# Kernel tuning notes

Measured on AMD Instinct MI355X. Metric: run time of the kernel, lower is better.

The kernel has to match this reference:

```python
import jax, jax.numpy as jnp
import numpy as np
from jax import lax

N_CLASS = 21          # VOC: 20 foreground + background
SCORE_THRESH = 0.05   # 'evaluate' preset
NMS_THRESH = 0.3


def loc2bbox(src_bbox, loc):
    # src_bbox, loc: [N, 4] in (y1, x1, y2, x2) / (dy, dx, dh, dw)
    h = src_bbox[:, 2] - src_bbox[:, 0]
    w = src_bbox[:, 3] - src_bbox[:, 1]
    cy = src_bbox[:, 0] + 0.5 * h
    cx = src_bbox[:, 1] + 0.5 * w
    dy, dx, dh, dw = loc[:, 0], loc[:, 1], loc[:, 2], loc[:, 3]
    ncy = dy * h + cy
    ncx = dx * w + cx
    nh = jnp.exp(dh) * h
    nw = jnp.exp(dw) * w
    return jnp.stack([ncy - 0.5 * nh, ncx - 0.5 * nw,
                      ncy + 0.5 * nh, ncx + 0.5 * nw], axis=1)


def pairwise_iou(boxes):
    # boxes: [R, 4] (y1, x1, y2, x2) -> [R, R]
    area = (boxes[:, 2] - boxes[:, 0]) * (boxes[:, 3] - boxes[:, 1])
    ty1 = jnp.maximum(boxes[:, None, 0], boxes[None, :, 0])
    tx1 = jnp.maximum(boxes[:, None, 1], boxes[None, :, 1])
    ty2 = jnp.minimum(boxes[:, None, 2], boxes[None, :, 2])
    tx2 = jnp.minimum(boxes[:, None, 3], boxes[None, :, 3])
    inter = jnp.clip(ty2 - ty1, 0) * jnp.clip(tx2 - tx1, 0)
    union = area[:, None] + area[None, :] - inter
    return inter / jnp.maximum(union, 1e-10)


def nms_keep(boxes, scores):
    # boxes [R,4], scores [R] for one class. Returns bool keep mask [R]
    # (score-thresholded + greedy NMS), fixed shape (mask instead of gather).
    R = boxes.shape[0]
    valid = scores > SCORE_THRESH
    order = jnp.argsort(-scores)
    b = boxes[order]
    v = valid[order]
    suppress = pairwise_iou(b) > NMS_THRESH  # [R, R]
    idx = jnp.arange(R)

    def body(i, keep):
        sup_by_earlier = jnp.any(keep & suppress[:, i] & (idx < i))
        return keep.at[i].set(v[i] & ~sup_by_earlier)

    keep_sorted = lax.fori_loop(0, R, body, jnp.zeros((R,), bool))
    return jnp.zeros((R,), bool).at[order].set(keep_sorted)


def setup_inputs() -> dict:
    key = jax.random.key(0)
    k1, k2, k3, k4 = jax.random.split(key, 4)
    R = 2000
    size_h, size_w = 600, 800
    roi_cls_loc = jax.random.normal(k1, (R, N_CLASS * 4), jnp.float32)
    roi_scores = jax.random.normal(k2, (R, N_CLASS), jnp.float32)
    # valid (y1, x1, y2, x2) rois inside the image
    yx = jax.random.uniform(k3, (R, 2), jnp.float32) * jnp.array([size_h - 32.0, size_w - 32.0])
    hw = 16.0 + jax.random.uniform(k4, (R, 2), jnp.float32) * 128.0
    rois = jnp.concatenate([yx, yx + hw], axis=1)
    return {"roi_cls_loc": roi_cls_loc, "roi_scores": roi_scores,
            "rois": rois, "size_h": size_h, "size_w": size_w}


def reference(roi_cls_loc, roi_scores, rois, size_h, size_w):
    R = rois.shape[0]
    mean = jnp.tile(jnp.asarray([0.0, 0.0, 0.0, 0.0], roi_cls_loc.dtype), N_CLASS)
    std = jnp.tile(jnp.asarray([0.1, 0.1, 0.2, 0.2], roi_cls_loc.dtype), N_CLASS)
    loc = roi_cls_loc * std + mean                      # [R, 4*C]
    loc = loc.reshape(R * N_CLASS, 4)
    src = jnp.broadcast_to(rois[:, None, :], (R, N_CLASS, 4)).reshape(R * N_CLASS, 4)
    box = loc2bbox(src, loc).reshape(R, N_CLASS, 4)
    # clamp y coords (0,2) to [0, H], x coords (1,3) to [0, W]
    y = jnp.clip(box[..., 0::2], 0.0, float(size_h))
    x = jnp.clip(box[..., 1::2], 0.0, float(size_w))
    box = jnp.stack([y[..., 0], x[..., 0], y[..., 1], x[..., 1]], axis=-1)
    prob = jax.nn.softmax(roi_scores, axis=1)           # [R, C]
    # foreground classes only (skip background class 0)
    cls_box = jnp.transpose(box[:, 1:, :], (1, 0, 2))   # [C-1, R, 4]
    cls_prob = prob[:, 1:].T                            # [C-1, R]
    keep = jax.vmap(nms_keep)(lax.stop_gradient(cls_box),
                              lax.stop_gradient(cls_prob))  # [C-1, R] bool
    kept = keep.astype(box.dtype)[..., None]
    # fixed-shape detections: per-class boxes + score, zeroed where suppressed
    out = jnp.concatenate([cls_box * kept, cls_prob[..., None] * kept], axis=-1)
    return out  # [C-1, R, 5]
```

## Files before the change

### kernel.cpp

```cpp
#include <hip/hip_runtime.h>
#include <math.h>

#define NCLS 21
#define NCO 20
#define SUB 12
#define TPB 256
#define RCAP 2048
#define RMAX 2000
#define SEGW 256
#define LDSW 7680
#define SCORE_THRESH 0.05f

typedef unsigned long long u64;
typedef unsigned int u32;
typedef unsigned short u16;

#define IOU_MID (20132661.0 / 67108864.0)

__device__ __forceinline__ u64 readlane64(u64 v, int l) {
    u32 lo = (u32)__builtin_amdgcn_readlane((int)(u32)v, l);
    u32 hi = (u32)__builtin_amdgcn_readlane((int)(u32)(v >> 32), l);
    return ((u64)hi << 32) | lo;
}
__device__ __forceinline__ float readlanef(float v, int l) {
    return __uint_as_float((u32)__builtin_amdgcn_readlane((int)__float_as_uint(v), l));
}
__device__ __forceinline__ u64 shflxor64(u64 v, int m) {
    u32 lo = (u32)__shfl_xor((int)(u32)v, m, 64);
    u32 hi = (u32)__shfl_xor((int)(u32)(v >> 32), m, 64);
    return ((u64)hi << 32) | lo;
}

__device__ __forceinline__ int coff(int ic, int nw) {
    return ((ic * nw - ((ic * (ic - 1)) >> 1)) << 6);
}

__device__ __forceinline__ void decode_box(
    const float* __restrict__ rois, const float* __restrict__ loc,
    int r, int cls, float sh, float sw,
    float& by1, float& bx1, float& by2, float& bx2)
{
    float4 rb = *(const float4*)(rois + r * 4);
    float y1 = rb.x, x1 = rb.y, y2 = rb.z, x2 = rb.w;
    float h = y2 - y1, w = x2 - x1;
    float cy = y1 + 0.5f * h, cx = x1 + 0.5f * w;
    float4 l4 = *(const float4*)(loc + r * (NCLS * 4) + cls * 4);
    float dy = l4.x * 0.1f, dx = l4.y * 0.1f;
    float dh = l4.z * 0.2f, dw = l4.w * 0.2f;
    float ncy = dy * h + cy, ncx = dx * w + cx;
    float nh = expf(dh) * h, nw = expf(dw) * w;
    by1 = fminf(fmaxf(ncy - 0.5f * nh, 0.f), sh);
    bx1 = fminf(fmaxf(ncx - 0.5f * nw, 0.f), sw);
    by2 = fminf(fmaxf(ncy + 0.5f * nh, 0.f), sh);
    bx2 = fminf(fmaxf(ncx + 0.5f * nw, 0.f), sw);
}

__device__ __forceinline__ float softmax_p(
    const float* __restrict__ scores, int r, int cls)
{
    const float* srow = scores + r * NCLS;
    float s[NCLS];
    float4 a0 = *(const float4*)(srow);
    float4 a1 = *(const float4*)(srow + 4);
    float4 a2 = *(const float4*)(srow + 8);
    float4 a3 = *(const float4*)(srow + 12);
    float4 a4 = *(const float4*)(srow + 16);
    s[0]=a0.x; s[1]=a0.y; s[2]=a0.z; s[3]=a0.w;
    s[4]=a1.x; s[5]=a1.y; s[6]=a1.z; s[7]=a1.w;
    s[8]=a2.x; s[9]=a2.y; s[10]=a2.z; s[11]=a2.w;
    s[12]=a3.x; s[13]=a3.y; s[14]=a3.z; s[15]=a3.w;
    s[16]=a4.x; s[17]=a4.y; s[18]=a4.z; s[19]=a4.w;
    s[20]=srow[20];
    float m = -INFINITY;
#pragma unroll
    for (int k = 0; k < NCLS; ++k) m = fmaxf(m, s[k]);
    float sum = 0.f, ec = 0.f;
#pragma unroll
    for (int k = 0; k < NCLS; ++k) {
        float e = expf(s[k] - m);
        sum += e;
        if (k == cls) ec = e;
    }
    return ec / sum;
}

__global__ __launch_bounds__(TPB) void keygen_kernel(
    const float* __restrict__ scores, u64* __restrict__ ukey,
    int* __restrict__ cntA, int R)
{
    __shared__ u64 lkey[TPB];
    __shared__ int cnt;
    const int t = threadIdx.x;
    const int c = blockIdx.x / SUB;
    const int s = blockIdx.x % SUB;
    const int lane = t & 63;
    if (t == 0) cnt = 0;
    __syncthreads();
    const int rpb = (R + SUB - 1) / SUB;
    const int r0 = s * rpb, r1 = min(R, r0 + rpb);
    for (int r = r0 + t; r < r1; r += TPB) {
        float p = softmax_p(scores, r, c + 1);
        bool valid = (p > SCORE_THRESH);
        u64 key = ((u64)(~__float_as_uint(p)) << 32) | (u32)r;
        u64 bal = __ballot(valid);
        if (bal) {
            int nb = (int)__popcll(bal);
            int base = 0;
            if (lane == 0) base = atomicAdd(&cnt, nb);
            base = __shfl(base, 0, 64);
            if (valid)
                lkey[base + (int)__popcll(bal & ((1ull << lane) - 1ull))] = key;
        }
    }
    __syncthreads();
    const int n = cnt;
    if (t == 0) cntA[(c << 4) | s] = n;
    for (int j = t; j < n; j += TPB)
        ukey[(size_t)c * (SUB * SEGW) + s * SEGW + j] = lkey[j];
}

__global__ __launch_bounds__(512) void rank_kernel(
    const float* __restrict__ loc, const float* __restrict__ rois,
    const int* __restrict__ ph, const int* __restrict__ pw,
    const u64* __restrict__ ukey, const int* __restrict__ cntA,
    u64* __restrict__ ord, int* __restrict__ nvv,
    float4* __restrict__ pbG, float* __restrict__ arG, int R)
{
    __shared__ __align__(16) u64 vkey[RCAP + 2];
    const int t = threadIdx.x;
    const int c = blockIdx.x / SUB;
    const int s = blockIdx.x % SUB;
    const int wv = t >> 6, lane = t & 63;
    int nv = 0;
    int baseA = 0, nA = 0, baseB = 0, nB = 0;
#pragma unroll
    for (int k = 0; k < SUB; ++k) {
        int ck = cntA[(c << 4) | k];
        if (k < wv)     baseA += ck;
        if (k == wv)    nA = ck;
        if (k < wv + 8) baseB += ck;
        if (k == wv + 8) nB = ck;
        nv += ck;
    }
    for (int j = lane; j < nA; j += 64)
        vkey[baseA + j] = ukey[(size_t)c * (SUB * SEGW) + wv * SEGW + j];
    if (wv + 8 < SUB)
        for (int j = lane; j < nB; j += 64)
            vkey[baseB + j] = ukey[(size_t)c * (SUB * SEGW) + (wv + 8) * SEGW + j];
    if (t == 0) vkey[nv] = ~0ull;
    __syncthreads();

    const int sl = (nv + SUB - 1) / SUB;
    const int i0 = s * sl;
    const int nmy = max(0, min(nv - i0, sl));
    const int q = t & 3;
    const ulonglong2* vk2 = (const ulonglong2*)vkey;
    const int nj2 = (nv + 1) >> 1;
    const int jb0 = (q * nj2) >> 2;
    const int jb1 = ((q + 1) * nj2) >> 2;
    const float shf = (float)(*ph), swf = (float)(*pw);
    for (int il = (t >> 2); il < nmy; il += 128) {
        u64 kk = vkey[i0 + il];
        int rank = 0;
#pragma unroll 8
        for (int j = jb0; j < jb1; ++j) {
            ulonglong2 kj = vk2[j];
            rank += (int)(kj.x < kk) + (int)(kj.y < kk);
        }
        rank += __shfl_xor(rank, 1, 64);
        rank += __shfl_xor(rank, 2, 64);
        if (q == 0) {
            int r = (int)(u32)kk;
            float b0, b1, b2, b3;
            decode_box(rois, loc, r, c + 1, shf, swf, b0, b1, b2, b3);
            ord[((size_t)c << 11) + rank] = kk;
            pbG[((size_t)c << 11) + rank] = make_float4(b0, b1, b2, b3);
            arG[((size_t)c << 11) + rank] = (b2 - b0) * (b3 - b1);
        }
    }
    if (t == 0 && s == 0) nvv[c] = nv;
}

__global__ __launch_bounds__(512) void maskp_kernel(
    const float4* __restrict__ pbG, const float* __restrict__ arG,
    const int* __restrict__ nvv, u64* __restrict__ M)
{
    __shared__ float4 pb[RCAP];
    __shared__ float ar[RCAP];
    const int t = threadIdx.x;
    const int c = blockIdx.x / SUB;
    const int s = blockIdx.x % SUB;
    const int lane = t & 63;
    const int nv = nvv[c];
    const int nw = (nv + 63) >> 6;
    for (int i = t; i < nv; i += 512) {
        pb[i] = pbG[((size_t)c << 11) + i];
        ar[i] = arG[((size_t)c << 11) + i];
    }
    __syncthreads();

    const int wid = (s << 3) | (t >> 6);
    const int ntasks = nw * (nw + 1) / 2;
    u64* Mc = M + ((size_t)c << 16);
    for (int task = wid; task < ntasks; task += SUB * 8) {
        int ic = 0, rm = task;
        while (rm >= nw - ic) { rm -= nw - ic; ++ic; }
        int v = ic + rm;
        int i = (ic << 6) + lane;
        float4 a = pb[i];
        float iarea = ar[i];
        float4 rj = pb[(v << 6) + lane];
        float ja_l = ar[(v << 6) + lane];
        int jcnt = min(64, nv - (v << 6));
        u64 m = 0;
        for (int jj = 0; jj < jcnt; ++jj) {
            float jy1 = readlanef(rj.x, jj);
            float jx1 = readlanef(rj.y, jj);
            float jy2 = readlanef(rj.z, jj);
            float jx2 = readlanef(rj.w, jj);
            float ja  = readlanef(ja_l, jj);
            float ty1 = fmaxf(a.x, jy1);
            float tx1 = fmaxf(a.y, jx1);
            float ty2 = fminf(a.z, jy2);
            float tx2 = fminf(a.w, jx2);
            float inter = fmaxf(ty2 - ty1, 0.f) * fmaxf(tx2 - tx1, 0.f);
            float uni = fmaxf(iarea + ja - inter, 1e-10f);
            if ((double)inter > IOU_MID * (double)uni) m |= 1ull << jj;
        }
        if (v == ic) m &= (lane < 63) ? (~0ull << (lane + 1)) : 0ull;
        int W = nw - ic;
        if (i < nv) Mc[coff(ic, nw) + lane * W + (v - ic)] = m;
    }
}

__global__ __launch_bounds__(TPB) void resolveout_kernel(
    const float* __restrict__ loc, const float* __restrict__ rois,
    const int* __restrict__ ph, const int* __restrict__ pw,
    const u64* __restrict__ ord, const int* __restrict__ nvv,
    const u64* __restrict__ M, float* __restrict__ out, int R)
{
    __shared__ u64 mlds[LDSW];
    __shared__ u64 keptw[32];
    const int t = threadIdx.x;
    const int c = blockIdx.x / SUB;
    const int s = blockIdx.x % SUB;
    const int nv = nvv[c];
    const int nw = (nv + 63) >> 6;
    const u64* Mc = M + ((size_t)c << 16);
    const int S = coff(nw, nw);
    const bool lds_ok = (S <= LDSW);
    if (t < 32) keptw[t] = 0;

    if (lds_ok) {
        for (int base = 0; base < S; base += 2048) {
            u64 v[8];
#pragma unroll
            for (int j = 0; j < 8; ++j) {
                int k = base + (j << 8) + t;
                v[j] = (k < S) ? Mc[k] : 0ull;
            }
#pragma unroll
            for (int j = 0; j < 8; ++j) {
                int k = base + (j << 8) + t;
                if (k < S) mlds[k] = v[j];
            }
        }
    }
    __syncthreads();

    if (t < 64) {
        const int lane = t;
        auto core = [&](const auto* B) {
            u64 remreg = 0;
            for (int w = 0; w < nw; ++w) {
                const int W = nw - w;
                const int cb = coff(w, nw);
                int i = (w << 6) + lane;
                u64 cw = (i < nv) ? B[cb + lane * W] : 0ull;
                int remn = nv - (w << 6);
                u64 vb = (remn >= 64) ? ~0ull : ((1ull << remn) - 1ull);
                u64 cand = vb & ~readlane64(remreg, w);
                u64 X = cand;
                if (X) {
                    for (int it = 0; it < 64; ++it) {
                        u64 contrib = ((X >> lane) & 1ull) ? cw : 0ull;
#pragma unroll
                        for (int d = 1; d < 64; d <<= 1)
                            contrib |= shflxor64(contrib, d);
                        bool keep = ((cand >> lane) & 1ull) &&
                                    !((contrib >> lane) & 1ull);
                        u64 Xn = __ballot(keep);
                        if (Xn == X) break;
                        X = Xn;
                    }
                    if (lane == 0) keptw[w] = X;
                    bool lact = (lane > w) && (lane < nw);
                    u64 km = X, acc = 0;
                    while (km) {
                        int bs[8];
#pragma unroll
                        for (int g = 0; g < 8; ++g) {
                            bs[g] = km ? (__ffsll(km) - 1) : -1;
                            if (km) km &= km - 1;
                        }
                        u64 tmp[8];
#pragma unroll
                        for (int g = 0; g < 8; ++g)
                            tmp[g] = (bs[g] >= 0 && lact)
                                ? B[cb + bs[g] * W + (lane - w)] : 0ull;
#pragma unroll
                        for (int g = 0; g < 8; ++g) acc |= tmp[g];
                    }
                    if (lact) remreg |= acc;
                }
            }
        };
        if (lds_ok) core(mlds); else core(Mc);
    }
    __syncthreads();

    const int chunk = (R + SUB - 1) / SUB;
    const int r0 = s * chunk;
    const int r1 = min(R, r0 + chunk);
    float* slice = out + (size_t)c * R * 5;
    for (int k = r0 * 5 + t; k < r1 * 5; k += TPB) slice[k] = 0.f;
    __syncthreads();

    const float sh = (float)(*ph), sw = (float)(*pw);
    for (int i = t; i < nv; i += TPB) {
        if ((keptw[i >> 6] >> (i & 63)) & 1ull) {
            u64 key = ord[((size_t)c << 11) + i];
            int r = (int)(u32)key;
            if (r >= r0 && r < r1) {
                float v0, v1, v2, v3;
                decode_box(rois, loc, r, c + 1, sh, sw, v0, v1, v2, v3);
                float* p = slice + (size_t)r * 5;
                p[0] = v0; p[1] = v1; p[2] = v2; p[3] = v3;
                p[4] = __uint_as_float(~(u32)(key >> 32));
            }
        }
    }
}

#define NTH 1024
__global__ __launch_bounds__(NTH) void fused_kernel(
    const float* __restrict__ loc, const float* __restrict__ scores,
    const float* __restrict__ rois, const int* __restrict__ ph,
    const int* __restrict__ pw, float* __restrict__ out, int R)
{
    __shared__ u64 vkey[RMAX];
    __shared__ float2 p1[RMAX], p2[RMAX];
    __shared__ u64 chunk[64 * 33];
    __shared__ u64 rem[32];
    __shared__ int cnt;

    const int t = threadIdx.x;
    const int lane = t & 63;
    const int c = blockIdx.x + 1;
    const float sh = (float)(*ph), sw = (float)(*pw);

    if (t == 0) cnt = 0;
    if (t < 32) rem[t] = 0;
    __syncthreads();

    for (int r = t; r < R; r += NTH) {
        float p = softmax_p(scores, r, c);
        if (p > SCORE_THRESH) {
            int j = atomicAdd(&cnt, 1);
            vkey[j] = ((u64)(~__float_as_uint(p)) << 32) | (u32)r;
        }
    }
    __syncthreads();
    const int nv = cnt;
    const int nw = (nv + 63) >> 6;

    u64 kk0 = 0, kk1 = 0;
    int r0 = 0, r1 = 0;
    bool in0 = (t < nv), in1 = (t + NTH < nv);
    if (in0) kk0 = vkey[t];
    if (in1) kk1 = vkey[t + NTH];
#pragma unroll 8
    for (int i = 0; i < nv; ++i) {
        u64 k = vkey[i];
        r0 += (k < kk0);
        r1 += (k < kk1);
    }
    __syncthreads();

    for (int u = 0; u < 2; ++u) {
        bool act = u ? in1 : in0;
        if (act) {
            u64 kk = u ? kk1 : kk0;
            int rank = u ? r1 : r0;
            int r = (int)(kk & 0xffffffffu);
            float b0, b1, b2, b3;
            decode_box(rois, loc, r, c, sh, sw, b0, b1, b2, b3);
            vkey[rank] = kk;
            p1[rank] = make_float2(b0, b1);
            p2[rank] = make_float2(b2, b3);
        }
    }
    __syncthreads();

    for (int w = 0; w < nw; ++w) {
        int nwr = nw - w;
        u64 remw = rem[w];
        for (int task = t; task < (nwr << 6); task += NTH) {
            int vr = task >> 6, il = task & 63;
            int i = (w << 6) + il;
            u64 m = 0;
            if (i < nv && !((remw >> il) & 1ull)) {
                int v = w + vr;
                u64 rv = rem[v];
                if (~rv != 0ull) {
                    float2 a1 = p1[i], a2 = p2[i];
                    float iarea = (a2.x - a1.x) * (a2.y - a1.y);
                    int j0 = v << 6;
                    int jhi = min(64, nv - j0);
#pragma unroll 4
                    for (int jj = 0; jj < jhi; ++jj) {
                        float2 b1 = p1[j0 + jj], b2 = p2[j0 + jj];
                        float ty1 = fmaxf(a1.x, b1.x);
                        float tx1 = fmaxf(a1.y, b1.y);
                        float ty2 = fminf(a2.x, b2.x);
                        float tx2 = fminf(a2.y, b2.y);
                        float inter = fmaxf(ty2 - ty1, 0.f) * fmaxf(tx2 - tx1, 0.f);
                        float jarea = (b2.x - b1.x) * (b2.y - b1.y);
                        float uni = fmaxf(iarea + jarea - inter, 1e-10f);
                        if ((double)inter > IOU_MID * (double)uni) m |= 1ull << jj;
                    }
                    if (vr == 0)
                        m &= (il < 63) ? (~0ull << (il + 1)) : 0ull;
                }
            }
            chunk[il * 33 + vr] = m;
        }
        __syncthreads();

        u64 cand = chunk[lane * 33];
        u64 cur = rem[w];
        int remn = nv - (w << 6);
        u64 vb = (remn >= 64) ? ~0ull : ((1ull << remn) - 1ull);
        u64 avail = vb & ~cur;
        u64 kept = 0;
        while (avail) {
            int bb = __ffsll(avail) - 1;
            kept |= 1ull << bb;
            cur |= __shfl(cand, bb, 64);
            avail &= ~(cur | (1ull << bb));
        }
        int vr = t & 31, pg = t >> 5;
        if (vr >= 1 && vr < nwr) {
            u64 acc = 0, km = kept;
            int n = 0;
            while (km) {
                int bb = __ffsll(km) - 1;
                km &= km - 1;
                if ((n & 31) == pg) acc |= chunk[bb * 33 + vr];
                ++n;
            }
            if (acc) atomicOr(&rem[w + vr], acc);
        }
        if (t == 0) rem[w] = cur;
        __syncthreads();
    }

    u16* inv = (u16*)chunk;
    for (int r = t; r < R; r += NTH) inv[r] = 0xffffu;
    __syncthreads();
    for (int i = t; i < nv; i += NTH)
        if (!((rem[i >> 6] >> (i & 63)) & 1ull))
            inv[(int)(vkey[i] & 0xffffffffu)] = (u16)i;
    __syncthreads();
    float* slice = out + (size_t)(c - 1) * R * 5;
    for (int r = t; r < R; r += NTH) {
        int i = inv[r];
        float v0 = 0.f, v1 = 0.f, v2 = 0.f, v3 = 0.f, v4 = 0.f;
        if (i != 0xffff) {
            float2 a1 = p1[i], a2 = p2[i];
            v0 = a1.x; v1 = a1.y; v2 = a2.x; v3 = a2.y;
            v4 = __uint_as_float(~(u32)(vkey[i] >> 32));
        }
        float* p = slice + (size_t)r * 5;
        p[0] = v0; p[1] = v1; p[2] = v2; p[3] = v3; p[4] = v4;
    }
}

extern "C" void kernel_launch(void* const* d_in, const int* in_sizes, int n_in,
                              void* d_out, int out_size, void* d_ws, size_t ws_size,
                              hipStream_t stream) {
    const float* loc    = (const float*)d_in[0];
    const float* scores = (const float*)d_in[1];
    const float* rois   = (const float*)d_in[2];
    const int*   ph     = (const int*)d_in[3];
    const int*   pw     = (const int*)d_in[4];
    float* out = (float*)d_out;
    int R = in_sizes[2] / 4;

    size_t needM    = (size_t)NCO * RCAP * 32 * 8;
    size_t needOrd  = (size_t)NCO * RCAP * 8;
    size_t needUkey = (size_t)NCO * SUB * SEGW * 8;
    size_t needPbG  = (size_t)NCO * RCAP * 16;
    size_t needArG  = (size_t)NCO * RCAP * 4;
    size_t need     = needM + needOrd + needUkey + needPbG + needArG + 4096;

    if (R <= RCAP && R <= SUB * SEGW && ws_size >= need) {
        char* w     = (char*)d_ws;
        u64* M      = (u64*)w;                               w += needM;
        u64* ordp   = (u64*)w;                               w += needOrd;
        u64* ukey   = (u64*)w;                               w += needUkey;
        float4* pbG = (float4*)w;                            w += needPbG;
        float* arG  = (float*)w;                             w += needArG;
        int* cntA   = (int*)w;                               w += 2048;
        int* nvv    = (int*)w;

        keygen_kernel<<<NCO * SUB, TPB, 0, stream>>>(scores, ukey, cntA, R);
        rank_kernel<<<NCO * SUB, 512, 0, stream>>>(loc, rois, ph, pw, ukey,
                                                   cntA, ordp, nvv, pbG, arG, R);
        maskp_kernel<<<NCO * SUB, 512, 0, stream>>>(pbG, arG, nvv, M);
        resolveout_kernel<<<NCO * SUB, TPB, 0, stream>>>(loc, rois, ph, pw,
                                                         ordp, nvv, M, out, R);
    } else if (R <= RMAX) {
        fused_kernel<<<NCO, NTH, 0, stream>>>(loc, scores, rois, ph, pw, out, R);
    }
}
```

Measured before the change: 111.3 us.

## Fuse key generation and ranking into one per-class kernel

Merges the keygen and rank kernels into a single sortrank kernel that runs one 1024-thread block per class. Each block computes softmax keys straight into shared memory and then ranks them there. This drops one kernel launch and the global round-trip of per-segment keys and counts. In exchange, parallelism falls from 240 blocks to 20, so the softmax and the quadratic rank computation for each class run on a single CU.

```diff
diff --git a/kernel.cpp b/kernel.cpp
--- a/kernel.cpp
+++ b/kernel.cpp
@@ -7,7 +7,6 @@
 #define TPB 256
 #define RCAP 2048
 #define RMAX 2000
-#define SEGW 256
 #define LDSW 7680
 #define SCORE_THRESH 0.05f
 
@@ -84,21 +83,22 @@
     return ec / sum;
 }
 
-__global__ __launch_bounds__(TPB) void keygen_kernel(
-    const float* __restrict__ scores, u64* __restrict__ ukey,
-    int* __restrict__ cntA, int R)
-{
-    __shared__ u64 lkey[TPB];
+__global__ __launch_bounds__(1024) void sortrank_kernel(
+    const float* __restrict__ loc, const float* __restrict__ scores,
+    const float* __restrict__ rois, const int* __restrict__ ph,
+    const int* __restrict__ pw, u64* __restrict__ ord,
+    int* __restrict__ nvv, float4* __restrict__ pbG,
+    float* __restrict__ arG, int R)
+{
+    __shared__ __align__(16) u64 vkey[RCAP + 2];
     __shared__ int cnt;
     const int t = threadIdx.x;
-    const int c = blockIdx.x / SUB;
-    const int s = blockIdx.x % SUB;
+    const int c = blockIdx.x;
     const int lane = t & 63;
     if (t == 0) cnt = 0;
     __syncthreads();
-    const int rpb = (R + SUB - 1) / SUB;
-    const int r0 = s * rpb, r1 = min(R, r0 + rpb);
-    for (int r = r0 + t; r < r1; r += TPB) {
+
+    for (int r = t; r < R; r += 1024) {
         float p = softmax_p(scores, r, c + 1);
         bool valid = (p > SCORE_THRESH);
         u64 key = ((u64)(~__float_as_uint(p)) << 32) | (u32)r;
@@ -109,58 +109,22 @@
             if (lane == 0) base = atomicAdd(&cnt, nb);
             base = __shfl(base, 0, 64);
             if (valid)
-                lkey[base + (int)__popcll(bal & ((1ull << lane) - 1ull))] = key;
-        }
-    }
-    __syncthreads();
-    const int n = cnt;
-    if (t == 0) cntA[(c << 4) | s] = n;
-    for (int j = t; j < n; j += TPB)
-        ukey[(size_t)c * (SUB * SEGW) + s * SEGW + j] = lkey[j];
-}
-
-__global__ __launch_bounds__(512) void rank_kernel(
-    const float* __restrict__ loc, const float* __restrict__ rois,
-    const int* __restrict__ ph, const int* __restrict__ pw,
-    const u64* __restrict__ ukey, const int* __restrict__ cntA,
-    u64* __restrict__ ord, int* __restrict__ nvv,
-    float4* __restrict__ pbG, float* __restrict__ arG, int R)
-{
-    __shared__ __align__(16) u64 vkey[RCAP + 2];
-    const int t = threadIdx.x;
-    const int c = blockIdx.x / SUB;
-    const int s = blockIdx.x % SUB;
-    const int wv = t >> 6, lane = t & 63;
-    int nv = 0;
-    int baseA = 0, nA = 0, baseB = 0, nB = 0;
-#pragma unroll
-    for (int k = 0; k < SUB; ++k) {
-        int ck = cntA[(c << 4) | k];
-        if (k < wv)     baseA += ck;
-        if (k == wv)    nA = ck;
-        if (k < wv + 8) baseB += ck;
-        if (k == wv + 8) nB = ck;
-        nv += ck;
-    }
-    for (int j = lane; j < nA; j += 64)
-        vkey[baseA + j] = ukey[(size_t)c * (SUB * SEGW) + wv * SEGW + j];
-    if (wv + 8 < SUB)
-        for (int j = lane; j < nB; j += 64)
-            vkey[baseB + j] = ukey[(size_t)c * (SUB * SEGW) + (wv + 8) * SEGW + j];
-    if (t == 0) vkey[nv] = ~0ull;
-    __syncthreads();
-
-    const int sl = (nv + SUB - 1) / SUB;
-    const int i0 = s * sl;
-    const int nmy = max(0, min(nv - i0, sl));
+                vkey[base + (int)__popcll(bal & ((1ull << lane) - 1ull))] = key;
+        }
+    }
+    __syncthreads();
+    const int nv = cnt;
+    if (t == 0) { vkey[nv] = ~0ull; nvv[c] = nv; }
+    __syncthreads();
+
     const int q = t & 3;
     const ulonglong2* vk2 = (const ulonglong2*)vkey;
     const int nj2 = (nv + 1) >> 1;
     const int jb0 = (q * nj2) >> 2;
     const int jb1 = ((q + 1) * nj2) >> 2;
     const float shf = (float)(*ph), swf = (float)(*pw);
-    for (int il = (t >> 2); il < nmy; il += 128) {
-        u64 kk = vkey[i0 + il];
+    for (int il = (t >> 2); il < nv; il += 256) {
+        u64 kk = vkey[il];
         int rank = 0;
 #pragma unroll 8
         for (int j = jb0; j < jb1; ++j) {
@@ -178,7 +142,6 @@
             arG[((size_t)c << 11) + rank] = (b2 - b0) * (b3 - b1);
         }
     }
-    if (t == 0 && s == 0) nvv[c] = nv;
 }
 
 __global__ __launch_bounds__(512) void maskp_kernel(
@@ -499,24 +462,20 @@
 
     size_t needM    = (size_t)NCO * RCAP * 32 * 8;
     size_t needOrd  = (size_t)NCO * RCAP * 8;
-    size_t needUkey = (size_t)NCO * SUB * SEGW * 8;
     size_t needPbG  = (size_t)NCO * RCAP * 16;
     size_t needArG  = (size_t)NCO * RCAP * 4;
-    size_t need     = needM + needOrd + needUkey + needPbG + needArG + 4096;
-
-    if (R <= RCAP && R <= SUB * SEGW && ws_size >= need) {
+    size_t need     = needM + needOrd + needPbG + needArG + 4096;
+
+    if (R <= RCAP && ws_size >= need) {
         char* w     = (char*)d_ws;
         u64* M      = (u64*)w;                               w += needM;
         u64* ordp   = (u64*)w;                               w += needOrd;
-        u64* ukey   = (u64*)w;                               w += needUkey;
         float4* pbG = (float4*)w;                            w += needPbG;
         float* arG  = (float*)w;                             w += needArG;
-        int* cntA   = (int*)w;                               w += 2048;
         int* nvv    = (int*)w;
 
-        keygen_kernel<<<NCO * SUB, TPB, 0, stream>>>(scores, ukey, cntA, R);
-        rank_kernel<<<NCO * SUB, 512, 0, stream>>>(loc, rois, ph, pw, ukey,
-                                                   cntA, ordp, nvv, pbG, arG, R);
+        sortrank_kernel<<<NCO, 1024, 0, stream>>>(loc, scores, rois, ph, pw,
+                                                  ordp, nvv, pbG, arG, R);
         maskp_kernel<<<NCO * SUB, 512, 0, stream>>>(pbG, arG, nvv, M);
         resolveout_kernel<<<NCO * SUB, TPB, 0, stream>>>(loc, rois, ph, pw,
                                                          ordp, nvv, M, out, R);
```

Measured after the change: 132.1 us. 1.19x slower.
